# Kernel tuning notes

Measured on AMD Instinct MI355X. Metric: run time of the kernel, lower is better.

The kernel has to match this reference:

```python
import jax, jax.numpy as jnp
import numpy as np

B, L, D, NH = 4, 1500, 512, 8
HD = D // NH
EPS = 1e-8            # F.normalize eps
PEPS = 1.1920929e-07  # torch clamp_probs eps for float32
TEMP = 1.0


def setup_inputs():
    key = jax.random.key(0)
    ks = jax.random.split(key, 12)
    s = 1.0 / np.sqrt(D)
    eye = jnp.eye(D, dtype=jnp.float32)
    return {
        "hidden": jax.random.normal(ks[0], (B, L, D), jnp.float32),
        "lengths": jnp.ones((B,), jnp.float32),
        "u_noise": jax.random.uniform(ks[1], (B, L), jnp.float32),
        "W1": jax.random.normal(ks[2], (D, D), jnp.float32) * s,
        "b1": jnp.zeros((D,), jnp.float32),
        "W2": jax.random.normal(ks[3], (D, D), jnp.float32) * s,
        "b2": jnp.zeros((D,), jnp.float32),
        "Wq": eye + jax.random.normal(ks[4], (D, D), jnp.float32) * 0.01,
        "Wk": eye + jax.random.normal(ks[5], (D, D), jnp.float32) * 0.01,
        "sim_bias": jnp.float32(0.098),
        "learned_query": jax.random.normal(ks[6], (D,), jnp.float32),
        "Wpk": eye + jax.random.normal(ks[7], (D, D), jnp.float32) * 0.01,
        "Wpv": eye + jax.random.normal(ks[8], (D, D), jnp.float32) * 0.01,
        "Wpo": eye + jax.random.normal(ks[9], (D, D), jnp.float32) * 0.01,
        "ln_g": jnp.ones((D,), jnp.float32),
        "ln_b": jnp.zeros((D,), jnp.float32),
    }


def reference(hidden, lengths, u_noise, W1, b1, W2, b2, Wq, Wk, sim_bias,
              learned_query, Wpk, Wpv, Wpo, ln_g, ln_b):
    Bb, Ll, Dd = hidden.shape

    def nrm(x):
        n = jnp.sqrt(jnp.sum(x * x, -1, keepdims=True))
        return x / jnp.maximum(n, EPS)

    def mlp(x):
        return jax.nn.gelu(x @ W1.T + b1, approximate=False) @ W2.T + b2

    # boundary logits from adjacent-frame cosine similarity (dropout = eval identity)
    q_in = nrm(hidden[:, :-1]); q = nrm(mlp(q_in) + q_in) @ Wq.T
    k_in = nrm(hidden[:, 1:]);  k = nrm(mlp(k_in) + k_in) @ Wk.T
    cos = jnp.sum(q * k, -1)                                   # (B, L-1)
    probs = jnp.clip((1.0 - (cos + sim_bias)) * 0.5, 0.0, 1.0)
    probs = jnp.pad(probs, ((0, 0), (0, 1)))                   # (B, L)

    # RelaxedBernoulli rsample with explicit logistic noise
    p = jnp.clip(probs, PEPS, 1.0 - PEPS)
    u = jnp.clip(u_noise, PEPS, 1.0 - PEPS)
    soft = jax.nn.sigmoid((jnp.log(p) - jnp.log1p(-p) + jnp.log(u) - jnp.log1p(-u)) / TEMP)
    hard = (soft > 0.5).astype(hidden.dtype)

    idx = jnp.arange(Ll)
    valid_len = jnp.minimum((lengths * (Ll + 1)).astype(jnp.int32) - 1, Ll)
    trunc = (valid_len < Ll)[:, None]
    zmask = trunc & (idx[None] >= valid_len[:, None])
    omask = trunc & (idx[None] == valid_len[:, None])
    soft = jnp.where(omask, 1.0, jnp.where(zmask, 0.0, soft))
    hard = jnp.where(omask, 1.0, jnp.where(zmask, 0.0, hard))
    hard_b = hard - jax.lax.stop_gradient(soft) + soft         # straight-through
    # emergency boundary for all-zero rows
    no_b = (jnp.sum(hard, 1) == 0)[:, None]
    hard_b = jnp.where(no_b & (idx[None] == jnp.minimum(valid_len, Ll - 1)[:, None]), 1.0, hard_b)

    # segment membership (common()): token l in segment s iff exclusive cumsum == s
    seg = jnp.cumsum(hard_b, 1) - hard_b                       # (B, L)
    lmask = idx[None] < (lengths * Ll).astype(jnp.int32)[:, None]
    seg_mask = (seg[:, :, None] == idx[None, None, :].astype(hidden.dtype)) & lmask[:, :, None]  # (B,L,S)

    # layernorm + K/V projections
    mu = jnp.mean(hidden, -1, keepdims=True)
    hv = hidden - mu
    hn = hv / jnp.sqrt(jnp.mean(hv * hv, -1, keepdims=True) + 1e-5) * ln_g + ln_b
    keys = (hn @ Wpk.T).reshape(Bb, Ll, NH, HD)
    vals = (hn @ Wpv.T).reshape(Bb, Ll, NH, HD)

    # query is shared across segments -> scores only differ via the segment mask
    qh = learned_query.reshape(NH, HD)
    base = jnp.einsum('hd,blhd->bhl', qh, keys) * (HD ** -0.5)  # (B,H,L)
    mask_t = jnp.transpose(seg_mask, (0, 2, 1))[:, None]        # (B,1,S,L)
    sc = jnp.where(mask_t, base[:, :, None, :], -jnp.inf)       # (B,H,S,L)
    aw = jnp.nan_to_num(jax.nn.softmax(sc, axis=-1))            # empty segments -> 0 rows
    pooled = jnp.einsum('bhsl,blhd->bshd', aw, vals).reshape(Bb, Ll, Dd)
    return pooled @ Wpo.T                                       # (B, S=L, D)
```

## Files before the change

kernel.cpp:

```cpp
#include <hip/hip_runtime.h>
#include <math.h>

#define Bz 4
#define Lz 1500
#define Dz 512
#define NHz 8
#define Nz (Bz*Lz)
#define PEPSf 1.1920929e-07f

typedef __bf16 bf16x8 __attribute__((ext_vector_type(8)));
typedef unsigned short u16x8 __attribute__((ext_vector_type(8)));
typedef float f32x4 __attribute__((ext_vector_type(4)));
typedef unsigned short us;

__device__ __forceinline__ us f2bf(float f) {
  unsigned u = __float_as_uint(f);
  return (us)((u + 0x7fffu + ((u >> 16) & 1u)) >> 16);
}
__device__ __forceinline__ float bf2f(us b) {
  return __uint_as_float(((unsigned)b) << 16);
}
__device__ __forceinline__ int ti_idx(int row, int col) {
  return (((row >> 4) * 64 + (col >> 3)) << 7) + ((row & 15) << 3) + (col & 7);
}
__device__ __forceinline__ void st_tiled(us* __restrict__ P, int row, int col, us v) {
  P[ti_idx(row, col)] = v;
}

__device__ __forceinline__ bool decode_blk(int bx, int ncg, int& R, int& cg) {
  int xcd = bx & 7, v = bx >> 3;
  cg = v % ncg;
  R = (v / ncg) * 8 + xcd;
  return R < 94;
}

__global__ __launch_bounds__(256) void k_prep(
    const float* __restrict__ hidden,
    const float* __restrict__ g, const float* __restrict__ bb,
    const float* __restrict__ s0, const float* __restrict__ s1, const float* __restrict__ s2,
    const float* __restrict__ s3,
    const float* __restrict__ Wq, const float* __restrict__ Wk,
    const float* __restrict__ Wpk, const float* __restrict__ lq,
    us* __restrict__ h0, us* __restrict__ h1, us* __restrict__ h2, us* __restrict__ h3,
    us* __restrict__ l0, us* __restrict__ l1,
    us* __restrict__ WkTh, us* __restrict__ WkTl, us* __restrict__ WqTh, us* __restrict__ WqTl,
    us* __restrict__ wqeh, us* __restrict__ wqel,
    us* __restrict__ Uh, us* __restrict__ Ul, us* __restrict__ HNh, us* __restrict__ HNl) {
  const int t = threadIdx.x;
  if (blockIdx.x < 288) {
    const int u = blockIdx.x, rt = u & 31, mat = u >> 5;
    if (mat == 8) {
      if (rt < 8) {
        for (int d = t; d < Dz; d += 256) {
          float acc = 0.f;
          for (int e = 0; e < 64; ++e)
            acc += lq[rt * 64 + e] * Wpk[(size_t)(rt * 64 + e) * Dz + d];
          us hb = f2bf(acc);
          st_tiled(wqeh, rt, d, hb);
          st_tiled(wqel, rt, d, f2bf(acc - bf2f(hb)));
        }
      }
      return;
    }
    const float* S; us* H; us* L = nullptr; bool tr = false;
    switch (mat) {
      case 0: S = s0; H = h0; L = l0; break;
      case 1: S = s1; H = h1; L = l1; break;
      case 2: S = s2; H = h2; break;
      case 3: S = s3; H = h3; break;
      case 4: S = Wk; H = WkTh; L = WkTl; tr = true; break;
      default: S = Wq; H = WqTh; L = WqTl; tr = true; break;
    }
    for (int e = t; e < 8192; e += 256) {
      int mm = e >> 9, c = e & 511;
      float x = tr ? S[(size_t)c * 512 + (rt * 16 + mm)]
                   : S[(size_t)(rt * 16 + mm) * 512 + c];
      us hb = f2bf(x);
      int off = ((rt * 64 + (c >> 3)) << 7) + (mm << 3) + (c & 7);
      H[off] = hb;
      if (L) L[off] = f2bf(x - bf2f(hb));
    }
    return;
  }
  const int rb = blockIdx.x - 288;
  const int rl = t >> 4, sub = t & 15;
  const int row = rb * 16 + rl;
  __shared__ float gs[Dz], bs[Dz];
  gs[t] = g[t]; gs[t + 256] = g[t + 256];
  bs[t] = bb[t]; bs[t + 256] = bb[t + 256];
  __syncthreads();
  const f32x4* xp = (const f32x4*)(hidden + (size_t)row * Dz + sub * 32);
  f32x4 xv[8];
  #pragma unroll
  for (int i = 0; i < 8; ++i) xv[i] = xp[i];
  float s = 0.f, q = 0.f;
  #pragma unroll
  for (int i = 0; i < 8; ++i)
    #pragma unroll
    for (int j = 0; j < 4; ++j) { float v = xv[i][j]; s += v; q += v * v; }
  #pragma unroll
  for (int o = 1; o < 16; o <<= 1) { s += __shfl_xor(s, o, 16); q += __shfl_xor(q, o, 16); }
  float un = 1.f / fmaxf(sqrtf(q), 1e-8f);
  float mu = s * (1.f / 512.f);
  float var = fmaxf(q * (1.f / 512.f) - mu * mu, 0.f);
  float r = rsqrtf(var + 1e-5f);
  const int rowoff = rl << 3;
  #pragma unroll
  for (int ch = 0; ch < 4; ++ch) {
    const int c0 = sub * 32 + ch * 8;
    u16x8 uh, ul, hh, hl;
    #pragma unroll
    for (int k = 0; k < 8; ++k) {
      float xx = xv[ch * 2 + (k >> 2)][k & 3];
      float u = xx * un;
      us b = f2bf(u);
      uh[k] = b; ul[k] = f2bf(u - bf2f(b));
      float hn = (xx - mu) * r * gs[c0 + k] + bs[c0 + k];
      us nb = f2bf(hn);
      hh[k] = nb; hl[k] = f2bf(hn - bf2f(nb));
    }
    const int off = ((rb * 64 + sub * 4 + ch) << 7) + rowoff;
    *(u16x8*)(Uh + off) = uh;
    *(u16x8*)(Ul + off) = ul;
    *(u16x8*)(HNh + off) = hh;
    *(u16x8*)(HNl + off) = hl;
  }
}

template<int SPLIT>
__device__ __forceinline__ void gemm_body(
    const us* __restrict__ Ah, const us* __restrict__ Al,
    const us* __restrict__ Bh, const us* __restrict__ Bl,
    const float* __restrict__ bias,
    const us* __restrict__ addH, const us* __restrict__ addL, int doGelu,
    float* __restrict__ outF, us* __restrict__ outR,
    us* __restrict__ outH, us* __restrict__ outL, float* __restrict__ outBase,
    int R, int cg, int colbase, int Nrows) {
  const int t = threadIdx.x, w = t >> 6, l = t & 63;
  const int m = l & 15, q = l >> 4;
  const int wr = w & 1, wc = w >> 1;
  const int laneoff = q * 128 + m * 8;
  const int nrtm1 = (Nrows >> 4) - 1;

  const u16x8* pa[2]; const u16x8* pal[2];
  const u16x8* pb[2]; const u16x8* pbl[2];
  #pragma unroll
  for (int i = 0; i < 2; ++i) {
    int rt = min(R * 4 + wr * 2 + i, nrtm1);
    pa[i] = (const u16x8*)(Ah + (size_t)rt * 8192 + laneoff);
    if (SPLIT == 3) pal[i] = (const u16x8*)(Al + (size_t)rt * 8192 + laneoff);
  }
  #pragma unroll
  for (int j = 0; j < 2; ++j) {
    int ct = cg * 4 + wc * 2 + j;
    pb[j] = (const u16x8*)(Bh + (size_t)ct * 8192 + laneoff);
    if (SPLIT == 3) pbl[j] = (const u16x8*)(Bl + (size_t)ct * 8192 + laneoff);
  }

  u16x8 bAh[2][2], bAl[2][2], bBh[2][2], bBl[2][2];
  #pragma unroll
  for (int i = 0; i < 2; ++i) {
    bAh[0][i] = pa[i][0];
    if (SPLIT == 3) bAl[0][i] = pal[i][0];
  }
  #pragma unroll
  for (int j = 0; j < 2; ++j) {
    bBh[0][j] = pb[j][0];
    if (SPLIT == 3) bBl[0][j] = pbl[j][0];
  }

  f32x4 acc[2][2];
  #pragma unroll
  for (int i = 0; i < 2; ++i)
    #pragma unroll
    for (int j = 0; j < 2; ++j) acc[i][j] = (f32x4){0.f, 0.f, 0.f, 0.f};

  #pragma unroll 2
  for (int s = 0; s < 16; ++s) {
    const int cur = s & 1, nxt = cur ^ 1;
    const int sn = (s + 1) & 15;
    #pragma unroll
    for (int i = 0; i < 2; ++i) {
      bAh[nxt][i] = pa[i][sn * 64];
      if (SPLIT == 3) bAl[nxt][i] = pal[i][sn * 64];
    }
    #pragma unroll
    for (int j = 0; j < 2; ++j) {
      bBh[nxt][j] = pb[j][sn * 64];
      if (SPLIT == 3) bBl[nxt][j] = pbl[j][sn * 64];
    }
    #pragma unroll
    for (int i = 0; i < 2; ++i)
      #pragma unroll
      for (int j = 0; j < 2; ++j) {
        bf16x8 a = __builtin_bit_cast(bf16x8, bAh[cur][i]);
        bf16x8 b = __builtin_bit_cast(bf16x8, bBh[cur][j]);
        acc[i][j] = __builtin_amdgcn_mfma_f32_16x16x32_bf16(a, b, acc[i][j], 0, 0, 0);
        if (SPLIT == 3) {
          bf16x8 al_ = __builtin_bit_cast(bf16x8, bAl[cur][i]);
          bf16x8 bl_ = __builtin_bit_cast(bf16x8, bBl[cur][j]);
          acc[i][j] = __builtin_amdgcn_mfma_f32_16x16x32_bf16(a, bl_, acc[i][j], 0, 0, 0);
          acc[i][j] = __builtin_amdgcn_mfma_f32_16x16x32_bf16(al_, b, acc[i][j], 0, 0, 0);
        }
      }
  }

  const int row0 = R * 64 + wr * 32;
  const int col0 = colbase + wc * 32;
  #pragma unroll
  for (int i = 0; i < 2; ++i) {
    #pragma unroll
    for (int r = 0; r < 4; ++r) {
      const int grow = row0 + i * 16 + q * 4 + r;
      if (grow >= Nrows) continue;
      #pragma unroll
      for (int j = 0; j < 2; ++j) {
        const int gcol = col0 + j * 16 + m;
        float v = acc[i][j][r];
        if (outBase) {
          if (gcol < NHz) outBase[(size_t)grow * NHz + gcol] = v * 0.125f;
          continue;
        }
        if (bias)   v += bias[gcol];
        if (addH) {
          int ai = ti_idx(grow, gcol);
          v += bf2f(addH[ai]) + bf2f(addL[ai]);
        }
        if (doGelu) v = 0.5f * v * (1.f + erff(v * 0.70710678118654752f));
        if (outF) outF[(size_t)grow * Dz + gcol] = v;
        if (outR) outR[(size_t)grow * Dz + gcol] = f2bf(v);
        if (outH) {
          us hb = f2bf(v);
          st_tiled(outH, grow, gcol, hb);
          if (outL) st_tiled(outL, grow, gcol, f2bf(v - bf2f(hb)));
        }
      }
    }
  }
}

__global__ __launch_bounds__(256, 4) void g_phase2(
    const us* Uh, const us* Ul, const us* W1h, const us* W1l, const float* b1, us* T1h, us* T1l,
    const us* HNh, const us* HNl, const us* Wpvh, us* VALSb,
    const us* WkTh, const us* WkTl, const us* WqTh, const us* WqTl, us* Gth, us* Gtl,
    const us* wqeh, const us* wqel, float* base) {
  const int u = blockIdx.x;
  if (u < 768) {
    int R, c;
    if (decode_blk(u, 8, R, c))
      gemm_body<3>(Uh, Ul, W1h, W1l, b1, nullptr, nullptr, 1,
                   nullptr, nullptr, T1h, T1l, nullptr, R, c, c * 64, Nz);
    return;
  }
  if (u < 1536) {
    int R, c;
    if (decode_blk(u - 768, 8, R, c))
      gemm_body<1>(HNh, nullptr, Wpvh, nullptr, nullptr, nullptr, nullptr, 0,
                   nullptr, VALSb, nullptr, nullptr, nullptr, R, c, c * 64, Nz);
    return;
  }
  if (u < 1600) {
    int bx = u - 1536;
    gemm_body<3>(WkTh, WkTl, WqTh, WqTl, nullptr, nullptr, nullptr, 0,
                 nullptr, nullptr, Gth, Gtl, nullptr, bx >> 3, bx & 7, (bx & 7) * 64, 512);
    return;
  }
  {
    int R = u - 1600;
    if (R < 94)
      gemm_body<3>(HNh, HNl, wqeh, wqel, nullptr, nullptr, nullptr, 0,
                   nullptr, nullptr, nullptr, nullptr, base, R, 0, 0, Nz);
  }
}

__global__ __launch_bounds__(256, 4) void g_w2(
    const us* T1h, const us* T1l, const us* W2h, const us* W2l, const float* b2,
    const us* Uh, const us* Ul, float* M, us* Mh, us* Ml) {
  int R, cg;
  if (!decode_blk(blockIdx.x, 8, R, cg)) return;
  gemm_body<3>(T1h, T1l, W2h, W2l, b2, Uh, Ul, 0, M, nullptr, Mh, Ml, nullptr,
               R, cg, cg * 64, Nz);
}

__global__ __launch_bounds__(256, 4) void g_p(
    const us* Mh, const us* Ml, const us* Gth, const us* Gtl, float* P) {
  int R, cg;
  if (!decode_blk(blockIdx.x, 8, R, cg)) return;
  gemm_body<3>(Mh, Ml, Gth, Gtl, nullptr, nullptr, nullptr, 0,
               P, nullptr, nullptr, nullptr, nullptr, R, cg, cg * 64, Nz);
}

__global__ __launch_bounds__(256, 4) void g_out(
    const us* Ph, const us* Wpoh, const int* __restrict__ segmeta, float* out) {
  int R, cg;
  if (!decode_blk(blockIdx.x, 8, R, cg)) return;
  const int r0 = R * 64, r1 = min(R * 64 + 63, Nz - 1);
  const int b0 = r0 / Lz, b1 = r1 / Lz;
  bool allz = true;
  for (int b = b0; b <= b1; ++b) {
    int smin = max(r0, b * Lz) - b * Lz;
    if (smin < segmeta[b * 2]) { allz = false; break; }
  }
  if (allz) {
    const int t = threadIdx.x;
    for (int e = t; e < 1024; e += 256) {
      int rr = e >> 4, cc = e & 15;
      int grow = r0 + rr;
      if (grow < Nz)
        *(f32x4*)(out + (size_t)grow * Dz + cg * 64 + cc * 4) = (f32x4){0.f, 0.f, 0.f, 0.f};
    }
    return;
  }
  gemm_body<1>(Ph, nullptr, Wpoh, nullptr, nullptr, nullptr, nullptr, 0,
               out, nullptr, nullptr, nullptr, nullptr, R, cg, cg * 64, Nz);
}

__global__ __launch_bounds__(256) void k_probs(const float* __restrict__ P,
    const float* __restrict__ M, const float* __restrict__ simb,
    float* __restrict__ probs) {
  const int w = threadIdx.x >> 6, t = threadIdx.x & 63;
  const int l = blockIdx.x * 4 + w, b = blockIdx.y;
  if (l >= Lz) return;
  if (l == Lz - 1) { if (t == 0) probs[(size_t)b * Lz + l] = 0.f; return; }
  const float* pp = P + ((size_t)b * Lz + l) * Dz;
  const float* m0 = M + ((size_t)b * Lz + l) * Dz;
  const float* m1 = M + ((size_t)b * Lz + l + 1) * Dz;
  float accd = 0.f, q0 = 0.f, q1 = 0.f;
  for (int i = t; i < Dz; i += 64) {
    float a = pp[i], x0 = m0[i], x1 = m1[i];
    accd += a * x1; q0 += x0 * x0; q1 += x1 * x1;
  }
  #pragma unroll
  for (int o = 32; o > 0; o >>= 1) {
    accd += __shfl_xor(accd, o, 64);
    q0 += __shfl_xor(q0, o, 64);
    q1 += __shfl_xor(q1, o, 64);
  }
  if (t == 0) {
    float un0 = 1.f / fmaxf(sqrtf(q0), 1e-8f);
    float un1 = 1.f / fmaxf(sqrtf(q1), 1e-8f);
    float cosv = accd * un0 * un1;
    float p = (1.f - (cosv + simb[0])) * 0.5f;
    probs[(size_t)b * Lz + l] = fminf(fmaxf(p, 0.f), 1.f);
  }
}

__global__ __launch_bounds__(256) void k_boundary(const float* __restrict__ probs,
    const float* __restrict__ un, const float* __restrict__ lengths,
    int* __restrict__ seg_start, int* __restrict__ seg_meta) {
  const int b = blockIdx.x, t = threadIdx.x;
  __shared__ float hard[Lz];
  __shared__ float ws4[4];
  __shared__ float wsum[4];
  const float len = lengths[b];
  const int valid_len = min((int)(len * (Lz + 1)) - 1, Lz);
  const int Lm = (int)(len * Lz);
  const bool trunc = valid_len < Lz;
  for (int l = t; l < Lz; l += 256) {
    float p = probs[(size_t)b * Lz + l];
    p = fminf(fmaxf(p, PEPSf), 1.f - PEPSf);
    float u = un[(size_t)b * Lz + l];
    u = fminf(fmaxf(u, PEPSf), 1.f - PEPSf);
    float z = logf(p) - log1pf(-p) + logf(u) - log1pf(-u);
    float soft = 1.f / (1.f + expf(-z));
    float hd = soft > 0.5f ? 1.f : 0.f;
    if (trunc && l >= valid_len) hd = (l == valid_len) ? 1.f : 0.f;
    hard[l] = hd;
  }
  __syncthreads();
  float sm = 0.f;
  for (int l = t; l < Lz; l += 256) sm += hard[l];
  #pragma unroll
  for (int o = 32; o > 0; o >>= 1) sm += __shfl_xor(sm, o, 64);
  if ((t & 63) == 0) ws4[t >> 6] = sm;
  __syncthreads();
  float total = ws4[0] + ws4[1] + ws4[2] + ws4[3];
  if (total == 0.f && t == 0) hard[min(valid_len, Lz - 1)] = 1.f;
  __syncthreads();
  const int l0 = t * 6;
  float loc = 0.f;
  for (int i = 0; i < 6; ++i) { int l = l0 + i; if (l < Lz) loc += hard[l]; }
  const int wid = t >> 6, lane = t & 63;
  float v = loc;
  #pragma unroll
  for (int o = 1; o < 64; o <<= 1) {
    float n = __shfl_up(v, o, 64);
    if (lane >= o) v += n;
  }
  if (lane == 63) wsum[wid] = v;
  __syncthreads();
  float woff = 0.f;
  for (int ww = 0; ww < wid; ++ww) woff += wsum[ww];
  float run = v + woff - loc;
  for (int i = 0; i < 6; ++i) {
    int l = l0 + i; if (l >= Lz) break;
    int seg = (int)(run + 0.5f);
    if (l == 0) seg_start[b * (Lz + 1) + 0] = 0;
    else if (hard[l - 1] > 0.5f) seg_start[b * (Lz + 1) + seg] = l;
    if (l == Lz - 1) {
      int nseg = seg + 1;
      seg_meta[b * 2 + 0] = nseg;
      seg_meta[b * 2 + 1] = Lm;
      seg_start[b * (Lz + 1) + nseg] = Lz;
    }
    run += hard[l];
  }
}

__global__ __launch_bounds__(256) void k_pool(const float* __restrict__ base,
    const us* __restrict__ VALSb, const int* __restrict__ seg_start,
    const int* __restrict__ seg_meta, us* __restrict__ Ph) {
  const int s = blockIdx.x, b = blockIdx.y, t = threadIdx.x;
  const int orow = b * Lz + s;
  const int nseg = seg_meta[b * 2], Lm = seg_meta[b * 2 + 1];
  int start = 0, end = 0;
  bool empty = true;
  if (s < nseg) {
    start = seg_start[b * (Lz + 1) + s];
    end = min(seg_start[b * (Lz + 1) + s + 1], Lm);
    empty = start >= end;
  }
  if (empty) { st_tiled(Ph, orow, t, 0); st_tiled(Ph, orow, t + 256, 0); return; }
  const int h = t >> 5, lane = t & 31;
  const float* bp = base + (size_t)b * Lz * NHz + h;
  float m = -1e30f;
  for (int l = start + lane; l < end; l += 32) m = fmaxf(m, bp[(size_t)l * NHz]);
  #pragma unroll
  for (int o = 16; o > 0; o >>= 1) m = fmaxf(m, __shfl_xor(m, o, 32));
  float den = 0.f;
  for (int l = start + lane; l < end; l += 32) den += expf(bp[(size_t)l * NHz] - m);
  #pragma unroll
  for (int o = 16; o > 0; o >>= 1) den += __shfl_xor(den, o, 32);
  float a0 = 0.f, a1 = 0.f;
  const us* vp = VALSb + (size_t)b * Lz * Dz + h * 64 + lane;
  for (int l = start; l < end; ++l) {
    float wgt = expf(bp[(size_t)l * NHz] - m);
    a0 += wgt * bf2f(vp[(size_t)l * Dz]);
    a1 += wgt * bf2f(vp[(size_t)l * Dz + 32]);
  }
  float inv = 1.f / den;
  st_tiled(Ph, orow, h * 64 + lane, f2bf(a0 * inv));
  st_tiled(Ph, orow, h * 64 + lane + 32, f2bf(a1 * inv));
}

extern "C" void kernel_launch(void* const* d_in, const int* in_sizes, int n_in,
                              void* d_out, int out_size, void* d_ws, size_t ws_size,
                              hipStream_t stream) {
  const float* hidden  = (const float*)d_in[0];
  const float* lengths = (const float*)d_in[1];
  const float* unoise  = (const float*)d_in[2];
  const float* W1  = (const float*)d_in[3];
  const float* b1  = (const float*)d_in[4];
  const float* W2  = (const float*)d_in[5];
  const float* b2  = (const float*)d_in[6];
  const float* Wq  = (const float*)d_in[7];
  const float* Wk  = (const float*)d_in[8];
  const float* simb   = (const float*)d_in[9];
  const float* lquery = (const float*)d_in[10];
  const float* Wpk = (const float*)d_in[11];
  const float* Wpv = (const float*)d_in[12];
  const float* Wpo = (const float*)d_in[13];
  const float* lng = (const float*)d_in[14];
  const float* lnb = (const float*)d_in[15];
  float* out = (float*)d_out;

  char* p = (char*)d_ws;
  const size_t SF = (size_t)Nz * Dz * 4;
  const size_t TP = (size_t)376 * 8192 * 2;
  const size_t WP = (size_t)32 * 8192 * 2;
  const size_t QP = (size_t)4 * 8192 * 2;
  float* M    = (float*)p; p += SF;
  float* PF   = (float*)p; p += SF;
  us* VALSb = (us*)p; p += TP;
  us* Uh  = (us*)p; p += TP;
  us* Ul  = (us*)p; p += TP;
  us* T1h = (us*)p; p += TP;
  us* T1l = (us*)p; p += TP;
  us* Mh  = (us*)p; p += TP;
  us* Ml  = (us*)p; p += TP;
  us* HNh = (us*)p; p += TP;
  us* HNl = (us*)p; p += TP;
  us* Ph  = (us*)p; p += TP;
  us* W1h = (us*)p; p += WP;
  us* W1l = (us*)p; p += WP;
  us* W2h = (us*)p; p += WP;
  us* W2l = (us*)p; p += WP;
  us* Wpvh = (us*)p; p += WP;
  us* Wpoh = (us*)p; p += WP;
  us* WkTh = (us*)p; p += WP;
  us* WkTl = (us*)p; p += WP;
  us* WqTh = (us*)p; p += WP;
  us* WqTl = (us*)p; p += WP;
  us* Gth  = (us*)p; p += WP;
  us* Gtl  = (us*)p; p += WP;
  us* wqeh = (us*)p; p += QP;
  us* wqel = (us*)p; p += QP;
  float* probs  = (float*)p; p += 24064;
  float* base   = (float*)p; p += 192000;
  int* segst    = (int*)p;   p += 24064;
  int* segmeta  = (int*)p;   p += 256;

  const int G8 = 8 * 12 * 8;

  k_prep<<<288 + 375, 256, 0, stream>>>(hidden, lng, lnb, W1, W2, Wpv, Wpo, Wq, Wk,
      Wpk, lquery, W1h, W2h, Wpvh, Wpoh, W1l, W2l, WkTh, WkTl, WqTh, WqTl,
      wqeh, wqel, Uh, Ul, HNh, HNl);
  g_phase2<<<1694, 256, 0, stream>>>(Uh, Ul, W1h, W1l, b1, T1h, T1l,
      HNh, HNl, Wpvh, VALSb, WkTh, WkTl, WqTh, WqTl, Gth, Gtl, wqeh, wqel, base);
  g_w2<<<G8, 256, 0, stream>>>(T1h, T1l, W2h, W2l, b2, Uh, Ul, M, Mh, Ml);
  g_p<<<G8, 256, 0, stream>>>(Mh, Ml, Gth, Gtl, PF);
  k_probs<<<dim3(375, Bz), 256, 0, stream>>>(PF, M, simb, probs);
  k_boundary<<<Bz, 256, 0, stream>>>(probs, unoise, lengths, segst, segmeta);
  k_pool<<<dim3(Lz, Bz), 256, 0, stream>>>(base, VALSb, segst, segmeta, Ph);
  g_out<<<G8, 256, 0, stream>>>(Ph, Wpoh, segmeta, out);
}
```

Baseline: 211.1 us.

## Fuse cosine-similarity reductions into GEMM epilogues and drop probs kernel

Squared norms of M are reduced per 32-column slice in the g_w2 epilogue, and the dot product of P with the next row of M is reduced in the g_p epilogue. This avoids writing the full fp32 P matrix and launching a separate k_probs kernel. k_boundary now sums 16 partial slices per row to form the cosine and probabilities. The cost is extra shuffles and strided reads of M in the g_p epilogue, plus more serial work inside the 4-block boundary kernel.

```diff
diff --git a/kernel.cpp b/kernel.cpp
--- a/kernel.cpp
+++ b/kernel.cpp
@@ -6,6 +6,7 @@
 #define Dz 512
 #define NHz 8
 #define Nz (Bz*Lz)
+#define NSL 6016
 #define PEPSf 1.1920929e-07f
 
 typedef __bf16 bf16x8 __attribute__((ext_vector_type(8)));
@@ -135,6 +136,7 @@
     const us* __restrict__ addH, const us* __restrict__ addL, int doGelu,
     float* __restrict__ outF, us* __restrict__ outR,
     us* __restrict__ outH, us* __restrict__ outL, float* __restrict__ outBase,
+    float* __restrict__ outNrm, float* __restrict__ outDot, const float* __restrict__ Mfull,
     int R, int cg, int colbase, int Nrows) {
   const int t = threadIdx.x, w = t >> 6, l = t & 63;
   const int m = l & 15, q = l >> 4;
@@ -207,12 +209,15 @@
 
   const int row0 = R * 64 + wr * 32;
   const int col0 = colbase + wc * 32;
+  const int slice = (colbase >> 5) + wc;
   #pragma unroll
   for (int i = 0; i < 2; ++i) {
     #pragma unroll
     for (int r = 0; r < 4; ++r) {
       const int grow = row0 + i * 16 + q * 4 + r;
       if (grow >= Nrows) continue;
+      float pn = 0.f, pd = 0.f;
+      const bool nd = outDot && ((grow % Lz) != (Lz - 1));
       #pragma unroll
       for (int j = 0; j < 2; ++j) {
         const int gcol = col0 + j * 16 + m;
@@ -234,6 +239,18 @@
           st_tiled(outH, grow, gcol, hb);
           if (outL) st_tiled(outL, grow, gcol, f2bf(v - bf2f(hb)));
         }
+        if (outNrm) pn += v * v;
+        if (nd) pd += v * Mfull[(size_t)(grow + 1) * Dz + gcol];
+      }
+      if (outNrm) {
+        #pragma unroll
+        for (int o = 8; o > 0; o >>= 1) pn += __shfl_xor(pn, o, 64);
+        if (m == 0) outNrm[(size_t)slice * NSL + grow] = pn;
+      }
+      if (outDot) {
+        #pragma unroll
+        for (int o = 8; o > 0; o >>= 1) pd += __shfl_xor(pd, o, 64);
+        if (m == 0) outDot[(size_t)slice * NSL + grow] = nd ? pd : 0.f;
       }
     }
   }
@@ -249,45 +266,51 @@
     int R, c;
     if (decode_blk(u, 8, R, c))
       gemm_body<3>(Uh, Ul, W1h, W1l, b1, nullptr, nullptr, 1,
-                   nullptr, nullptr, T1h, T1l, nullptr, R, c, c * 64, Nz);
+                   nullptr, nullptr, T1h, T1l, nullptr, nullptr, nullptr, nullptr,
+                   R, c, c * 64, Nz);
     return;
   }
   if (u < 1536) {
     int R, c;
     if (decode_blk(u - 768, 8, R, c))
       gemm_body<1>(HNh, nullptr, Wpvh, nullptr, nullptr, nullptr, nullptr, 0,
-                   nullptr, VALSb, nullptr, nullptr, nullptr, R, c, c * 64, Nz);
+                   nullptr, VALSb, nullptr, nullptr, nullptr, nullptr, nullptr, nullptr,
+                   R, c, c * 64, Nz);
     return;
   }
   if (u < 1600) {
     int bx = u - 1536;
     gemm_body<3>(WkTh, WkTl, WqTh, WqTl, nullptr, nullptr, nullptr, 0,
-                 nullptr, nullptr, Gth, Gtl, nullptr, bx >> 3, bx & 7, (bx & 7) * 64, 512);
+                 nullptr, nullptr, Gth, Gtl, nullptr, nullptr, nullptr, nullptr,
+                 bx >> 3, bx & 7, (bx & 7) * 64, 512);
     return;
   }
   {
     int R = u - 1600;
     if (R < 94)
       gemm_body<3>(HNh, HNl, wqeh, wqel, nullptr, nullptr, nullptr, 0,
-                   nullptr, nullptr, nullptr, nullptr, base, R, 0, 0, Nz);
+                   nullptr, nullptr, nullptr, nullptr, base, nullptr, nullptr, nullptr,
+                   R, 0, 0, Nz);
   }
 }
 
 __global__ __launch_bounds__(256, 4) void g_w2(
     const us* T1h, const us* T1l, const us* W2h, const us* W2l, const float* b2,
-    const us* Uh, const us* Ul, float* M, us* Mh, us* Ml) {
+    const us* Uh, const us* Ul, float* M, us* Mh, us* Ml, float* nrmpart) {
   int R, cg;
   if (!decode_blk(blockIdx.x, 8, R, cg)) return;
   gemm_body<3>(T1h, T1l, W2h, W2l, b2, Uh, Ul, 0, M, nullptr, Mh, Ml, nullptr,
-               R, cg, cg * 64, Nz);
+               nrmpart, nullptr, nullptr, R, cg, cg * 64, Nz);
 }
 
 __global__ __launch_bounds__(256, 4) void g_p(
-    const us* Mh, const us* Ml, const us* Gth, const us* Gtl, float* P) {
+    const us* Mh, const us* Ml, const us* Gth, const us* Gtl,
+    float* dotpart, const float* M) {
   int R, cg;
   if (!decode_blk(blockIdx.x, 8, R, cg)) return;
   gemm_body<3>(Mh, Ml, Gth, Gtl, nullptr, nullptr, nullptr, 0,
-               P, nullptr, nullptr, nullptr, nullptr, R, cg, cg * 64, Nz);
+               nullptr, nullptr, nullptr, nullptr, nullptr,
+               nullptr, dotpart, M, R, cg, cg * 64, Nz);
 }
 
 __global__ __launch_bounds__(256, 4) void g_out(
@@ -312,40 +335,13 @@
     return;
   }
   gemm_body<1>(Ph, nullptr, Wpoh, nullptr, nullptr, nullptr, nullptr, 0,
-               out, nullptr, nullptr, nullptr, nullptr, R, cg, cg * 64, Nz);
-}
-
-__global__ __launch_bounds__(256) void k_probs(const float* __restrict__ P,
-    const float* __restrict__ M, const float* __restrict__ simb,
-    float* __restrict__ probs) {
-  const int w = threadIdx.x >> 6, t = threadIdx.x & 63;
-  const int l = blockIdx.x * 4 + w, b = blockIdx.y;
-  if (l >= Lz) return;
-  if (l == Lz - 1) { if (t == 0) probs[(size_t)b * Lz + l] = 0.f; return; }
-  const float* pp = P + ((size_t)b * Lz + l) * Dz;
-  const float* m0 = M + ((size_t)b * Lz + l) * Dz;
-  const float* m1 = M + ((size_t)b * Lz + l + 1) * Dz;
-  float accd = 0.f, q0 = 0.f, q1 = 0.f;
-  for (int i = t; i < Dz; i += 64) {
-    float a = pp[i], x0 = m0[i], x1 = m1[i];
-    accd += a * x1; q0 += x0 * x0; q1 += x1 * x1;
-  }
-  #pragma unroll
-  for (int o = 32; o > 0; o >>= 1) {
-    accd += __shfl_xor(accd, o, 64);
-    q0 += __shfl_xor(q0, o, 64);
-    q1 += __shfl_xor(q1, o, 64);
-  }
-  if (t == 0) {
-    float un0 = 1.f / fmaxf(sqrtf(q0), 1e-8f);
-    float un1 = 1.f / fmaxf(sqrtf(q1), 1e-8f);
-    float cosv = accd * un0 * un1;
-    float p = (1.f - (cosv + simb[0])) * 0.5f;
-    probs[(size_t)b * Lz + l] = fminf(fmaxf(p, 0.f), 1.f);
-  }
-}
-
-__global__ __launch_bounds__(256) void k_boundary(const float* __restrict__ probs,
+               out, nullptr, nullptr, nullptr, nullptr, nullptr, nullptr, nullptr,
+               R, cg, cg * 64, Nz);
+}
+
+__global__ __launch_bounds__(256) void k_boundary(
+    const float* __restrict__ dotp, const float* __restrict__ nrmp,
+    const float* __restrict__ simb,
     const float* __restrict__ un, const float* __restrict__ lengths,
     int* __restrict__ seg_start, int* __restrict__ seg_meta) {
   const int b = blockIdx.x, t = threadIdx.x;
@@ -353,11 +349,28 @@
   __shared__ float ws4[4];
   __shared__ float wsum[4];
   const float len = lengths[b];
+  const float sb = simb[0];
   const int valid_len = min((int)(len * (Lz + 1)) - 1, Lz);
   const int Lm = (int)(len * Lz);
   const bool trunc = valid_len < Lz;
   for (int l = t; l < Lz; l += 256) {
-    float p = probs[(size_t)b * Lz + l];
+    float p;
+    if (l == Lz - 1) {
+      p = 0.f;
+    } else {
+      const size_t row = (size_t)b * Lz + l;
+      float d = 0.f, n0 = 0.f, n1 = 0.f;
+      #pragma unroll
+      for (int s = 0; s < 16; ++s) {
+        d  += dotp[(size_t)s * NSL + row];
+        n0 += nrmp[(size_t)s * NSL + row];
+        n1 += nrmp[(size_t)s * NSL + row + 1];
+      }
+      float un0 = 1.f / fmaxf(sqrtf(n0), 1e-8f);
+      float un1 = 1.f / fmaxf(sqrtf(n1), 1e-8f);
+      float cosv = d * un0 * un1;
+      p = fminf(fmaxf((1.f - (cosv + sb)) * 0.5f, 0.f), 1.f);
+    }
     p = fminf(fmaxf(p, PEPSf), 1.f - PEPSf);
     float u = un[(size_t)b * Lz + l];
     u = fminf(fmaxf(u, PEPSf), 1.f - PEPSf);
@@ -469,8 +482,8 @@
   const size_t TP = (size_t)376 * 8192 * 2;
   const size_t WP = (size_t)32 * 8192 * 2;
   const size_t QP = (size_t)4 * 8192 * 2;
+  const size_t DP = (size_t)16 * NSL * 4;
   float* M    = (float*)p; p += SF;
-  float* PF   = (float*)p; p += SF;
   us* VALSb = (us*)p; p += TP;
   us* Uh  = (us*)p; p += TP;
   us* Ul  = (us*)p; p += TP;
@@ -495,7 +508,8 @@
   us* Gtl  = (us*)p; p += WP;
   us* wqeh = (us*)p; p += QP;
   us* wqel = (us*)p; p += QP;
-  float* probs  = (float*)p; p += 24064;
+  float* dotpart = (float*)p; p += DP;
+  float* nrmpart = (float*)p; p += DP;
   float* base   = (float*)p; p += 192000;
   int* segst    = (int*)p;   p += 24064;
   int* segmeta  = (int*)p;   p += 256;
@@ -507,10 +521,10 @@
       wqeh, wqel, Uh, Ul, HNh, HNl);
   g_phase2<<<1694, 256, 0, stream>>>(Uh, Ul, W1h, W1l, b1, T1h, T1l,
       HNh, HNl, Wpvh, VALSb, WkTh, WkTl, WqTh, WqTl, Gth, Gtl, wqeh, wqel, base);
-  g_w2<<<G8, 256, 0, stream>>>(T1h, T1l, W2h, W2l, b2, Uh, Ul, M, Mh, Ml);
-  g_p<<<G8, 256, 0, stream>>>(Mh, Ml, Gth, Gtl, PF);
-  k_probs<<<dim3(375, Bz), 256, 0, stream>>>(PF, M, simb, probs);
-  k_boundary<<<Bz, 256, 0, stream>>>(probs, unoise, lengths, segst, segmeta);
+  g_w2<<<G8, 256, 0, stream>>>(T1h, T1l, W2h, W2l, b2, Uh, Ul, M, Mh, Ml, nrmpart);
+  g_p<<<G8, 256, 0, stream>>>(Mh, Ml, Gth, Gtl, dotpart, M);
+  k_boundary<<<Bz, 256, 0, stream>>>(dotpart, nrmpart, simb, unoise, lengths,
+      segst, segmeta);
   k_pool<<<dim3(Lz, Bz), 256, 0, stream>>>(base, VALSb, segst, segmeta, Ph);
   g_out<<<G8, 256, 0, stream>>>(Ph, Wpoh, segmeta, out);
 }
```

Measured after the change: 219.3 us. 1.04x slower.
